# Optimization experiments

Measured on AMD Instinct MI355X. Metric: run time of the kernel, lower is better.

The kernel has to match this reference:

```python
import jax, jax.numpy as jnp
import numpy as np

B, H, S, D = 2, 8, 2048, 64

def setup_inputs() -> dict:
    key = jax.random.key(0)
    ks = jax.random.split(key, 6)
    names = ["Qx", "Kx", "Vx", "Qy", "Ky", "Vy"]
    return {n: jax.random.normal(k, (B, H, S, D), dtype=jnp.float32)
            for n, k in zip(names, ks)}

def reference(Qx, Kx, Vx, Qy, Ky, Vy):
    scale = float(np.sqrt(Qx.shape[-1]))
    # Two score matmuls: [B,H,S,S] each
    ax = jnp.einsum('bhqd,bhkd->bhqk', Qx, Kx)
    ay = jnp.einsum('bhqd,bhkd->bhqk', Qy, Ky)
    # cat(dim=1) -> reshape(B,2,H,S,S) -> mean(dim=1) == elementwise average
    attn = (ax + ay) * 0.5
    # numerically stable softmax over keys; dropout is identity in eval mode
    w = jax.nn.softmax(attn / scale, axis=-1)
    # Shared attention weights into two value matmuls
    out1 = jnp.einsum('bhqk,bhkd->bhqd', w, Vx)
    out2 = jnp.einsum('bhqk,bhkd->bhqd', w, Vy)
    return (out1, out2)
```

## Files before the change

### kernel.cpp

```cpp
#include <hip/hip_runtime.h>
#include <hip/hip_bf16.h>

typedef __attribute__((ext_vector_type(4)))  float f32x4;
typedef __attribute__((ext_vector_type(16))) float f32x16;
typedef __attribute__((ext_vector_type(8)))  short s16x8;
typedef __attribute__((ext_vector_type(4)))  short s16x4;
typedef __attribute__((ext_vector_type(4)))  int   i32x4;

#define BB 2
#define HH 8
#define SS 2048
#define DD 64
#define QBLK 128
#define NT   32
#define NT2  16
#define NBH  (BB * HH)

#define WS_KX 0
#define WS_KY ((size_t)NBH * NT * 8192)
#define WS_VX ((size_t)2 * NBH * NT * 8192)
#define WS_VY ((size_t)3 * NBH * NT * 8192)
#define WS_NEED ((size_t)4 * NBH * NT * 8192)

__device__ __forceinline__ short f2bf(float x) {
    unsigned u = __builtin_bit_cast(unsigned, x);
    u = (u + 0x7FFFu + ((u >> 16) & 1u)) >> 16;
    return (short)u;
}

__device__ __forceinline__ unsigned cvtpk(float lo, float hi) {
    unsigned d;
    asm("v_cvt_pk_bf16_f32 %0, %1, %2" : "=v"(d) : "v"(lo), "v"(hi));
    return d;
}

__device__ __forceinline__ int swz(int row, int byteInRow) {
    return row * 128 + (byteInRow ^ ((row & 7) << 4));
}

__device__ __forceinline__ void glds16(const void* g, void* l) {
    __builtin_amdgcn_global_load_lds(
        (const __attribute__((address_space(1))) unsigned*)g,
        (__attribute__((address_space(3))) unsigned*)l, 16, 0, 0);
}

__global__ __launch_bounds__(256)
void prep_kv(const float* __restrict__ Kx, const float* __restrict__ Ky,
             const float* __restrict__ Vx, const float* __restrict__ Vy,
             char* __restrict__ ws)
{
    const int b = blockIdx.x;
    if (b < 1024) {
        const int tid  = b * 256 + threadIdx.x;
        const int dblk = tid & 7;
        const int s    = (tid >> 3) & 2047;
        const int bh   = tid >> 14;
        const size_t gi = ((size_t)bh * SS + s) * DD + dblk * 8;
        const int kt = s >> 6, row = s & 63;
        const size_t dst = (size_t)(bh * NT + kt) * 8192 + swz(row, dblk * 16);
        const float* px = Kx + gi;
        const float* py = Ky + gi;
        s16x8 a, bb;
#pragma unroll
        for (int i = 0; i < 8; ++i) { a[i] = f2bf(px[i]); bb[i] = f2bf(py[i]); }
        *(s16x8*)(ws + WS_KX + dst) = a;
        *(s16x8*)(ws + WS_KY + dst) = bb;
    } else {
        const int tid  = (b - 1024) * 256 + threadIdx.x;
        const int d    = tid & 63;
        const int sblk = (tid >> 6) & 7;
        const int kt   = (tid >> 9) & 31;
        const int bh   = tid >> 14;
        const size_t gbase = ((size_t)bh * SS + kt * 64 + sblk * 8) * DD + d;
        s16x8 a, bb;
#pragma unroll
        for (int i = 0; i < 8; ++i) {
            a[i]  = f2bf(Vx[gbase + (size_t)i * DD]);
            bb[i] = f2bf(Vy[gbase + (size_t)i * DD]);
        }
        const size_t dst = (size_t)(bh * NT + kt) * 8192 + swz(d, sblk * 16);
        *(s16x8*)(ws + WS_VX + dst) = a;
        *(s16x8*)(ws + WS_VY + dst) = bb;
    }
}

__global__ __launch_bounds__(512, 2)
void attn_main(const float* __restrict__ Qx, const float* __restrict__ Qy,
               const char* __restrict__ ws, float* __restrict__ Out)
{
    extern __shared__ char lds[];

    const int t    = threadIdx.x;
    const int lane = t & 63;
    const int w    = t >> 6;
    const int qsub = w & 3;
    const int ks   = w >> 2;
    const int l31  = lane & 31;
    const int hi   = lane >> 5;

    int bid = blockIdx.x;
    bid = (bid & 7) * 32 + (bid >> 3);
    const int bh = bid >> 4;
    const int q0 = (bid & 15) * QBLK;
    const size_t base = (size_t)bh * SS * DD;

    const float SCL = 0.09016844005556021f;

    const int qrow = q0 + qsub * 32 + l31;
    s16x8 qbx[4], qby[4];
#pragma unroll
    for (int dc = 0; dc < 4; ++dc) {
        const int d0 = dc * 16 + hi * 8;
        const float* qp = Qx + base + (size_t)qrow * DD + d0;
        const float* qq = Qy + base + (size_t)qrow * DD + d0;
        const float4 f0 = *(const float4*)qp;
        const float4 f1 = *(const float4*)(qp + 4);
        const float4 h0 = *(const float4*)qq;
        const float4 h1 = *(const float4*)(qq + 4);
        qbx[dc][0]=f2bf(f0.x*SCL); qbx[dc][1]=f2bf(f0.y*SCL); qbx[dc][2]=f2bf(f0.z*SCL); qbx[dc][3]=f2bf(f0.w*SCL);
        qbx[dc][4]=f2bf(f1.x*SCL); qbx[dc][5]=f2bf(f1.y*SCL); qbx[dc][6]=f2bf(f1.z*SCL); qbx[dc][7]=f2bf(f1.w*SCL);
        qby[dc][0]=f2bf(h0.x*SCL); qby[dc][1]=f2bf(h0.y*SCL); qby[dc][2]=f2bf(h0.z*SCL); qby[dc][3]=f2bf(h0.w*SCL);
        qby[dc][4]=f2bf(h1.x*SCL); qby[dc][5]=f2bf(h1.y*SCL); qby[dc][6]=f2bf(h1.z*SCL); qby[dc][7]=f2bf(h1.w*SCL);
    }

    f32x16 o1_0, o1_1, o2_0, o2_1;
#pragma unroll
    for (int j = 0; j < 16; ++j) { o1_0[j] = 0.f; o1_1[j] = 0.f; o2_0[j] = 0.f; o2_1[j] = 0.f; }
    float lsum = 0.f;

#define STAGE(kt_, b_)                                                             \
    do {                                                                           \
        const size_t img_ = (size_t)(bh * NT + (kt_) * 2) * 8192 + (size_t)t * 16; \
        char* dst_ = lds + (b_) * 65536 + t * 16;                                  \
        glds16(ws + WS_KX + img_,        dst_);                                    \
        glds16(ws + WS_KX + img_ + 8192, dst_ + 8192);                             \
        glds16(ws + WS_KY + img_,        dst_ + 16384);                            \
        glds16(ws + WS_KY + img_ + 8192, dst_ + 24576);                            \
        glds16(ws + WS_VX + img_,        dst_ + 32768);                            \
        glds16(ws + WS_VX + img_ + 8192, dst_ + 40960);                            \
        glds16(ws + WS_VY + img_,        dst_ + 49152);                            \
        glds16(ws + WS_VY + img_ + 8192, dst_ + 57344);                            \
    } while (0)

#define QK_BOTH(buf_, scA_, scB_)                                                  \
    do {                                                                           \
        const char* KxI_ = (buf_) + ks * 8192;                                     \
        const char* KyI_ = (buf_) + 16384 + ks * 8192;                             \
        _Pragma("unroll")                                                          \
        for (int dc = 0; dc < 4; ++dc) {                                           \
            const int offA = swz(l31,      dc * 32 + hi * 16);                     \
            const int offB = swz(32 + l31, dc * 32 + hi * 16);                     \
            const s16x8 ka0 = *(const s16x8*)(KxI_ + offA);                        \
            const s16x8 ka1 = *(const s16x8*)(KxI_ + offB);                        \
            const s16x8 kb0 = *(const s16x8*)(KyI_ + offA);                        \
            const s16x8 kb1 = *(const s16x8*)(KyI_ + offB);                        \
            scA_ = __builtin_amdgcn_mfma_f32_32x32x16_bf16(ka0, qbx[dc], scA_, 0, 0, 0); \
            scB_ = __builtin_amdgcn_mfma_f32_32x32x16_bf16(ka1, qbx[dc], scB_, 0, 0, 0); \
            scA_ = __builtin_amdgcn_mfma_f32_32x32x16_bf16(kb0, qby[dc], scA_, 0, 0, 0); \
            scB_ = __builtin_amdgcn_mfma_f32_32x32x16_bf16(kb1, qby[dc], scB_, 0, 0, 0); \
        }                                                                          \
    } while (0)

#define V_READS(buf_, h_, vr_)                                                     \
    do {                                                                           \
        const char* VxI_ = (buf_) + 32768 + ks * 8192;                             \
        const char* VyI_ = (buf_) + 49152 + ks * 8192;                             \
        _Pragma("unroll")                                                          \
        for (int ch = 0; ch < 2; ++ch) {                                           \
            const int off0 = swz(l31,      (h_) * 64 + ch * 32 + hi * 16);         \
            const int off1 = swz(32 + l31, (h_) * 64 + ch * 32 + hi * 16);         \
            vr_[ch * 4 + 0] = *(const s16x8*)(VxI_ + off0);                        \
            vr_[ch * 4 + 1] = *(const s16x8*)(VxI_ + off1);                        \
            vr_[ch * 4 + 2] = *(const s16x8*)(VyI_ + off0);                        \
            vr_[ch * 4 + 3] = *(const s16x8*)(VyI_ + off1);                        \
        }                                                                          \
    } while (0)

#define SOFTMAX_PA(sc_, pa_)                                                       \
    do {                                                                           \
        float s_ = 0.f;                                                            \
        _Pragma("unroll")                                                          \
        for (int j = 0; j < 16; ++j) { sc_[j] = exp2f(sc_[j]); s_ += sc_[j]; }     \
        lsum += s_;                                                                \
        _Pragma("unroll")                                                          \
        for (int ch = 0; ch < 2; ++ch) {                                           \
            const int b8 = ch * 8;                                                 \
            unsigned x0 = cvtpk(sc_[b8 + 0], sc_[b8 + 1]);                         \
            unsigned x1 = cvtpk(sc_[b8 + 2], sc_[b8 + 3]);                         \
            unsigned y0 = cvtpk(sc_[b8 + 4], sc_[b8 + 5]);                         \
            unsigned y1 = cvtpk(sc_[b8 + 6], sc_[b8 + 7]);                         \
            asm("v_permlane32_swap_b32 %0, %1" : "+v"(x0), "+v"(y0));              \
            asm("v_permlane32_swap_b32 %0, %1" : "+v"(x1), "+v"(y1));              \
            i32x4 pw;                                                              \
            pw[0] = (int)x0; pw[1] = (int)x1; pw[2] = (int)y0; pw[3] = (int)y1;    \
            pa_[ch] = __builtin_bit_cast(s16x8, pw);                               \
        }                                                                          \
    } while (0)

#define PV_BLOCK(pa_, vr_)                                                         \
    do {                                                                           \
        _Pragma("unroll")                                                          \
        for (int ch = 0; ch < 2; ++ch) {                                           \
            o1_0 = __builtin_amdgcn_mfma_f32_32x32x16_bf16(pa_[ch], vr_[ch*4+0], o1_0, 0, 0, 0); \
            o1_1 = __builtin_amdgcn_mfma_f32_32x32x16_bf16(pa_[ch], vr_[ch*4+1], o1_1, 0, 0, 0); \
            o2_0 = __builtin_amdgcn_mfma_f32_32x32x16_bf16(pa_[ch], vr_[ch*4+2], o2_0, 0, 0, 0); \
            o2_1 = __builtin_amdgcn_mfma_f32_32x32x16_bf16(pa_[ch], vr_[ch*4+3], o2_1, 0, 0, 0); \
        }                                                                          \
    } while (0)

#define ZERO16(v_) { _Pragma("unroll") for (int j = 0; j < 16; ++j) (v_)[j] = 0.f; }

    STAGE(0, 0);
    __syncthreads();
    int cur = 0;

    for (int kt = 0; kt < NT2; ++kt) {
        if (kt + 1 < NT2) STAGE(kt + 1, cur ^ 1);

        const char* buf = lds + cur * 65536;
        f32x16 scA, scB;
        ZERO16(scA); ZERO16(scB);
        s16x8 pa[2], vrA[8], vrB[8];

        __builtin_amdgcn_s_setprio(1);
        V_READS(buf, 0, vrA);
        V_READS(buf, 1, vrB);
        QK_BOTH(buf, scA, scB);
        SOFTMAX_PA(scA, pa);
        PV_BLOCK(pa, vrA);
        SOFTMAX_PA(scB, pa);
        PV_BLOCK(pa, vrB);
        __builtin_amdgcn_s_setprio(0);

        __syncthreads();
        cur ^= 1;
    }

#undef STAGE
#undef QK_BOTH
#undef V_READS
#undef SOFTMAX_PA
#undef PV_BLOCK
#undef ZERO16

    const float lh = lsum + __shfl_xor(lsum, 32);

    __syncthreads();
    float* ex   = (float*)lds;
    float* linv = (float*)(lds + 65536);
    const int exo = (qsub * 64 + lane) * 33;
    float* O1 = Out;
    float* O2 = Out + (size_t)BB * HH * SS * DD;

    if (ks == 1) {
#pragma unroll
        for (int j = 0; j < 16; ++j) { ex[exo + j] = o1_0[j]; ex[exo + 16 + j] = o1_1[j]; }
        ex[exo + 32] = lh;
    }
    __syncthreads();
    if (ks == 0 && hi == 0)
        linv[qsub * 32 + l31] = 1.0f / (lh + ex[exo + 32]);
    __syncthreads();
    if (ks == 0) {
#pragma unroll
        for (int j = 0; j < 16; ++j) {
            const int qr = (j & 3) + 8 * (j >> 2) + 4 * hi;
            const float invj = linv[qsub * 32 + qr];
            const size_t ob = base + (size_t)(q0 + qsub * 32 + qr) * DD + l31;
            O1[ob]      = (o1_0[j] + ex[exo + j])      * invj;
            O1[ob + 32] = (o1_1[j] + ex[exo + 16 + j]) * invj;
        }
    }
    __syncthreads();
    if (ks == 1) {
#pragma unroll
        for (int j = 0; j < 16; ++j) { ex[exo + j] = o2_0[j]; ex[exo + 16 + j] = o2_1[j]; }
    }
    __syncthreads();
    if (ks == 0) {
#pragma unroll
        for (int j = 0; j < 16; ++j) {
            const int qr = (j & 3) + 8 * (j >> 2) + 4 * hi;
            const float invj = linv[qsub * 32 + qr];
            const size_t ob = base + (size_t)(q0 + qsub * 32 + qr) * DD + l31;
            O2[ob]      = (o2_0[j] + ex[exo + j])      * invj;
            O2[ob + 32] = (o2_1[j] + ex[exo + 16 + j]) * invj;
        }
    }
}

__global__ __launch_bounds__(256, 2)
void attn_dual_fallback(const float* __restrict__ Qx, const float* __restrict__ Kx,
                        const float* __restrict__ Vx, const float* __restrict__ Qy,
                        const float* __restrict__ Ky, const float* __restrict__ Vy,
                        float* __restrict__ Out)
{
    __shared__ __attribute__((aligned(16))) char lds[40960];
    char* KxL  = lds;
    char* KyL  = lds + 8192;
    char* VtxL = lds + 16384;
    char* VtyL = lds + 24576;

    const int t    = threadIdx.x;
    const int lane = t & 63;
    const int w    = t >> 6;
    const int g    = lane >> 4;
    const int c    = lane & 15;
    char* PL = lds + 32768 + w * 2048;

    const int bid = blockIdx.x;
    const int bh  = bid >> 5;
    const int q0  = (bid & 31) * 64;
    const size_t base = (size_t)bh * SS * DD;

    const int qrowA = q0 + w * 16 + c;
    s16x8 qxf[2], qyf[2];
#pragma unroll
    for (int kk = 0; kk < 2; ++kk) {
        const int d0 = kk * 32 + g * 8;
        const float* qp = Qx + base + (size_t)qrowA * DD + d0;
        const float* qq = Qy + base + (size_t)qrowA * DD + d0;
#pragma unroll
        for (int i = 0; i < 8; ++i) { qxf[kk][i] = f2bf(qp[i]); qyf[kk][i] = f2bf(qq[i]); }
    }

    f32x4 o1[4], o2[4];
#pragma unroll
    for (int n = 0; n < 4; ++n) {
        o1[n] = (f32x4){0.f, 0.f, 0.f, 0.f};
        o2[n] = (f32x4){0.f, 0.f, 0.f, 0.f};
    }
    float m[4]    = {-1e30f, -1e30f, -1e30f, -1e30f};
    float lsum[4] = {0.f, 0.f, 0.f, 0.f};
    const float SCL = 0.09016844005556021f;

    for (int kt = 0; kt < SS / 64; ++kt) {
        __syncthreads();
#pragma unroll
        for (int j = 0; j < 4; ++j) {
            const int f   = t + 256 * j;
            const int row = f >> 4;
            const int c4  = f & 15;
            const size_t gi = base + (size_t)(kt * 64 + row) * DD + c4 * 4;
            const float4 kx = *(const float4*)(Kx + gi);
            const float4 ky = *(const float4*)(Ky + gi);
            const float4 vx = *(const float4*)(Vx + gi);
            const float4 vy = *(const float4*)(Vy + gi);
            s16x4 a; a[0]=f2bf(kx.x); a[1]=f2bf(kx.y); a[2]=f2bf(kx.z); a[3]=f2bf(kx.w);
            *(s16x4*)(KxL + swz(row, c4 * 8)) = a;
            s16x4 b; b[0]=f2bf(ky.x); b[1]=f2bf(ky.y); b[2]=f2bf(ky.z); b[3]=f2bf(ky.w);
            *(s16x4*)(KyL + swz(row, c4 * 8)) = b;
            const int d0 = c4 * 4;
            *(short*)(VtxL + swz(d0 + 0, row * 2)) = f2bf(vx.x);
            *(short*)(VtxL + swz(d0 + 1, row * 2)) = f2bf(vx.y);
            *(short*)(VtxL + swz(d0 + 2, row * 2)) = f2bf(vx.z);
            *(short*)(VtxL + swz(d0 + 3, row * 2)) = f2bf(vx.w);
            *(short*)(VtyL + swz(d0 + 0, row * 2)) = f2bf(vy.x);
            *(short*)(VtyL + swz(d0 + 1, row * 2)) = f2bf(vy.y);
            *(short*)(VtyL + swz(d0 + 2, row * 2)) = f2bf(vy.z);
            *(short*)(VtyL + swz(d0 + 3, row * 2)) = f2bf(vy.w);
        }
        __syncthreads();

        f32x4 sc[4];
#pragma unroll
        for (int n = 0; n < 4; ++n) {
            f32x4 acc = (f32x4){0.f, 0.f, 0.f, 0.f};
            const int keyrow = n * 16 + c;
#pragma unroll
            for (int kk = 0; kk < 2; ++kk) {
                const int off = swz(keyrow, (kk * 32 + g * 8) * 2);
                const s16x8 kxf = *(const s16x8*)(KxL + off);
                const s16x8 kyf = *(const s16x8*)(KyL + off);
                acc = __builtin_amdgcn_mfma_f32_16x16x32_bf16(qxf[kk], kxf, acc, 0, 0, 0);
                acc = __builtin_amdgcn_mfma_f32_16x16x32_bf16(qyf[kk], kyf, acc, 0, 0, 0);
            }
            sc[n] = acc;
        }

#pragma unroll
        for (int r = 0; r < 4; ++r) {
            float v0 = fmaxf(fmaxf(sc[0][r], sc[1][r]), fmaxf(sc[2][r], sc[3][r])) * SCL;
#pragma unroll
            for (int off = 1; off < 16; off <<= 1) v0 = fmaxf(v0, __shfl_xor(v0, off));
            const float mnew = fmaxf(m[r], v0);
            const float cr = exp2f(m[r] - mnew);
            m[r] = mnew;
            float srow = 0.f;
#pragma unroll
            for (int n = 0; n < 4; ++n) {
                const float pp = exp2f(sc[n][r] * SCL - mnew);
                srow += pp;
                *(short*)(PL + swz(g * 4 + r, (n * 16 + c) * 2)) = f2bf(pp);
            }
#pragma unroll
            for (int off = 1; off < 16; off <<= 1) srow += __shfl_xor(srow, off);
            lsum[r] = lsum[r] * cr + srow;
#pragma unroll
            for (int n = 0; n < 4; ++n) { o1[n][r] *= cr; o2[n][r] *= cr; }
        }

        s16x8 pf[2];
#pragma unroll
        for (int kk = 0; kk < 2; ++kk)
            pf[kk] = *(const s16x8*)(PL + swz(c, (kk * 32 + g * 8) * 2));
#pragma unroll
        for (int nd = 0; nd < 4; ++nd) {
            const int drow = nd * 16 + c;
#pragma unroll
            for (int kk = 0; kk < 2; ++kk) {
                const int off = swz(drow, (kk * 32 + g * 8) * 2);
                const s16x8 vxf = *(const s16x8*)(VtxL + off);
                const s16x8 vyf = *(const s16x8*)(VtyL + off);
                o1[nd] = __builtin_amdgcn_mfma_f32_16x16x32_bf16(pf[kk], vxf, o1[nd], 0, 0, 0);
                o2[nd] = __builtin_amdgcn_mfma_f32_16x16x32_bf16(pf[kk], vyf, o2[nd], 0, 0, 0);
            }
        }
    }

    float* O1 = Out;
    float* O2 = Out + (size_t)BB * HH * SS * DD;
#pragma unroll
    for (int r = 0; r < 4; ++r) {
        const float inv = 1.0f / lsum[r];
        const int qrow = q0 + w * 16 + g * 4 + r;
        const size_t ob = base + (size_t)qrow * DD + c;
#pragma unroll
        for (int nd = 0; nd < 4; ++nd) {
            O1[ob + nd * 16] = o1[nd][r] * inv;
            O2[ob + nd * 16] = o2[nd][r] * inv;
        }
    }
}

extern "C" void kernel_launch(void* const* d_in, const int* in_sizes, int n_in,
                              void* d_out, int out_size, void* d_ws, size_t ws_size,
                              hipStream_t stream) {
    const float* Qx = (const float*)d_in[0];
    const float* Kx = (const float*)d_in[1];
    const float* Vx = (const float*)d_in[2];
    const float* Qy = (const float*)d_in[3];
    const float* Ky = (const float*)d_in[4];
    const float* Vy = (const float*)d_in[5];
    float* Out = (float*)d_out;

    if (ws_size >= WS_NEED) {
        char* ws = (char*)d_ws;
        hipLaunchKernelGGL(prep_kv, dim3(2048), dim3(256), 0, stream,
                           Kx, Ky, Vx, Vy, ws);
        hipFuncSetAttribute((const void*)attn_main,
                            hipFuncAttributeMaxDynamicSharedMemorySize, 131072);
        hipLaunchKernelGGL(attn_main, dim3(NBH * (SS / QBLK)), dim3(512), 131072,
                           stream, Qx, Qy, (const char*)ws, Out);
    } else {
        hipLaunchKernelGGL(attn_dual_fallback, dim3(NBH * 32), dim3(256),
                           0, stream, Qx, Kx, Vx, Qy, Ky, Vy, Out);
    }
}
```

Baseline: 58.68 us.

## Software-pipeline QK and softmax/PV across iterations for ks==1 warps

Warps with ks==1 now compute QK scores for the next tile while running softmax and PV on the scores carried over from the previous tile, through a prologue and epilogue. Warps with ks==0 keep the original in-order schedule. The staggered phases are meant to let MFMA work from one warp group overlap softmax VALU work in the other and reduce contention. The cost is extra registers for the carried scores and V fragments, which may lower occupancy or cause spills.

```diff
diff --git a/kernel.cpp b/kernel.cpp
--- a/kernel.cpp
+++ b/kernel.cpp
@@ -210,30 +210,88 @@
 
 #define ZERO16(v_) { _Pragma("unroll") for (int j = 0; j < 16; ++j) (v_)[j] = 0.f; }
 
+    f32x16 scAc, scBc;
+    s16x8 vrAc[8], vrBc[8];
+    s16x8 pa[2];
+
     STAGE(0, 0);
     __syncthreads();
-    int cur = 0;
-
-    for (int kt = 0; kt < NT2; ++kt) {
+
+    {
+        STAGE(1, 1);
+        const char* buf = lds;
+        if (ks == 0) {
+            f32x16 scA, scB;
+            ZERO16(scA); ZERO16(scB);
+            s16x8 vrA[8], vrB[8];
+            __builtin_amdgcn_s_setprio(1);
+            V_READS(buf, 0, vrA);
+            V_READS(buf, 1, vrB);
+            QK_BOTH(buf, scA, scB);
+            SOFTMAX_PA(scA, pa);
+            PV_BLOCK(pa, vrA);
+            SOFTMAX_PA(scB, pa);
+            PV_BLOCK(pa, vrB);
+            __builtin_amdgcn_s_setprio(0);
+        } else {
+            ZERO16(scAc); ZERO16(scBc);
+            s16x8 vrA[8], vrB[8];
+            __builtin_amdgcn_s_setprio(1);
+            V_READS(buf, 0, vrA);
+            V_READS(buf, 1, vrB);
+            QK_BOTH(buf, scAc, scBc);
+            __builtin_amdgcn_s_setprio(0);
+#pragma unroll
+            for (int i = 0; i < 8; ++i) { vrAc[i] = vrA[i]; vrBc[i] = vrB[i]; }
+        }
+    }
+    __syncthreads();
+    int cur = 1;
+
+    for (int kt = 1; kt < NT2; ++kt) {
         if (kt + 1 < NT2) STAGE(kt + 1, cur ^ 1);
-
         const char* buf = lds + cur * 65536;
-        f32x16 scA, scB;
-        ZERO16(scA); ZERO16(scB);
-        s16x8 pa[2], vrA[8], vrB[8];
-
-        __builtin_amdgcn_s_setprio(1);
-        V_READS(buf, 0, vrA);
-        V_READS(buf, 1, vrB);
-        QK_BOTH(buf, scA, scB);
-        SOFTMAX_PA(scA, pa);
-        PV_BLOCK(pa, vrA);
-        SOFTMAX_PA(scB, pa);
-        PV_BLOCK(pa, vrB);
-        __builtin_amdgcn_s_setprio(0);
+
+        if (ks == 0) {
+            f32x16 scA, scB;
+            ZERO16(scA); ZERO16(scB);
+            s16x8 vrA[8], vrB[8];
+            __builtin_amdgcn_s_setprio(1);
+            V_READS(buf, 0, vrA);
+            V_READS(buf, 1, vrB);
+            QK_BOTH(buf, scA, scB);
+            SOFTMAX_PA(scA, pa);
+            PV_BLOCK(pa, vrA);
+            SOFTMAX_PA(scB, pa);
+            PV_BLOCK(pa, vrB);
+            __builtin_amdgcn_s_setprio(0);
+        } else {
+            __builtin_amdgcn_s_setprio(1);
+            SOFTMAX_PA(scAc, pa);
+            PV_BLOCK(pa, vrAc);
+            SOFTMAX_PA(scBc, pa);
+            PV_BLOCK(pa, vrBc);
+            ZERO16(scAc); ZERO16(scBc);
+            s16x8 vrA[8], vrB[8];
+            V_READS(buf, 0, vrA);
+            V_READS(buf, 1, vrB);
+            QK_BOTH(buf, scAc, scBc);
+            __builtin_amdgcn_s_setprio(0);
+#pragma unroll
+            for (int i = 0; i < 8; ++i) { vrAc[i] = vrA[i]; vrBc[i] = vrB[i]; }
+        }
 
         __syncthreads();
         cur ^= 1;
+    }
+
+    if (ks == 1) {
+        __builtin_amdgcn_s_setprio(1);
+        SOFTMAX_PA(scAc, pa);
+        PV_BLOCK(pa, vrAc);
+        SOFTMAX_PA(scBc, pa);
+        PV_BLOCK(pa, vrBc);
+        __builtin_amdgcn_s_setprio(0);
     }
 
 #undef STAGE
```

After: 145.2 us. 147% more time.
